# Performance work log

Measured on AMD Instinct MI355X. Metric: run time of the kernel, lower is better.

The kernel has to match this reference:

```python
import jax, jax.numpy as jnp
import numpy as np
import math

K = 32          # knn neighbors
NN = 32         # num_neighbor (kernel columns)
MAP = 32        # map_size
GROUP = 4
IN_C = 64
OUT_C = 64
EPS = 1e-5
TOPK = 3        # neighbors kept per kernel column in topkmax


def knn_idx(xc, k):
    # xc: [B,N,3]; returns indices of k nearest points (self included first)
    sq = -jnp.sum(xc * xc, axis=-1, keepdims=True)            # [B,N,1]
    pair = sq + 2.0 * jnp.einsum('bnd,bmd->bnm', xc, xc) + jnp.swapaxes(sq, 1, 2)
    return jax.lax.top_k(pair, k)[1]                          # [B,N,k]


def topkmax(p):
    # p: [M,k,NN]; keep top-TOPK along neighbor axis (dim=1), softmax over it
    pt = jnp.swapaxes(p, 1, 2)                                # [M,NN,k]
    thr = jax.lax.top_k(pt, TOPK)[0][..., -1:]
    pt = jnp.where(pt >= thr, pt, -1e10)
    return jnp.swapaxes(jax.nn.softmax(pt, axis=-1), 1, 2)


def setup_inputs() -> dict:
    key = jax.random.key(0)
    ks = jax.random.split(key, 8)
    B, N = 8, 2048
    in_c_x = IN_C // 2
    F = IN_C + in_c_x                                         # 96
    return {
        'x': jax.random.normal(ks[0], (B, 3, N), jnp.float32),
        'feature': jax.random.normal(ks[1], (B, IN_C, N), jnp.float32),
        'B_mat': jax.random.normal(ks[2], (7, MAP), jnp.float32),
        'kernels': jax.random.normal(ks[3], (3, NN), jnp.float32),
        'mlp_w': jax.random.normal(ks[4], (in_c_x, 2 * MAP), jnp.float32) * 0.1,
        'mlp_b': jnp.zeros((in_c_x,), jnp.float32),
        'conv_w': jax.random.normal(ks[5], (OUT_C, F * NN), jnp.float32) * 0.02,
        'conv_b': jnp.zeros((OUT_C,), jnp.float32),
        'bn_gamma': jnp.ones((OUT_C,), jnp.float32),
        'bn_beta': jnp.zeros((OUT_C,), jnp.float32),
    }


def reference(x, feature, B_mat, kernels, mlp_w, mlp_b, conv_w, conv_b, bn_gamma, bn_beta):
    bsz, in_c, n = feature.shape
    in_c_x = in_c // 2
    F = in_c + in_c_x
    M = bsz * n

    xc = jnp.swapaxes(x, 1, 2)                                # [B,N,3]
    idx = knn_idx(xc, K)                                      # [B,N,K]
    bix = jnp.arange(bsz)[:, None, None]

    x_neighs = xc[bix, idx].reshape(M, K, 3)                  # gather coords
    x_rep = jnp.broadcast_to(x_neighs[:, :1, :], x_neighs.shape)
    x_rel = x_neighs - x_rep
    x_dis = jnp.linalg.norm(x_rel, axis=-1, keepdims=True)

    # random Fourier features of [center, relative, distance]
    ff = (2.0 * math.pi) * jnp.concatenate([x_rep, x_rel, x_dis], -1) @ B_mat  # [M,K,MAP]
    ff = jnp.concatenate([jnp.sin(ff), jnp.cos(ff)], -1)                        # [M,K,2*MAP]
    x_feats = jnp.einsum('mki,oi->mok', ff, mlp_w) + mlp_b[None, :, None]       # [M,in_c_x,K]

    fN = jnp.swapaxes(feature, 1, 2)                          # [B,N,C]
    feats = fN[bix, idx].reshape(M, K, in_c)                  # gather features
    feats = jnp.swapaxes(feats, 1, 2)                         # [M,C,K]
    feats = jnp.concatenate([feats, x_feats], axis=1)         # [M,F,K]

    one_pad = jnp.zeros((K, NN), feature.dtype).at[0, 0].set(1.0)
    perm = topkmax(jnp.einsum('mkd,dn->mkn', x_rel, kernels) + one_pad)  # [M,K,NN]

    # group channel shuffle (F > 3 + in_c_x holds for in_c=64)
    feats = feats.reshape(M, GROUP, F // GROUP, K).transpose(0, 2, 1, 3).reshape(M, F, K)
    feats = jnp.einsum('mfk,mkn->mfn', feats, perm).reshape(M, F * NN)

    out = (feats @ conv_w.T + conv_b).reshape(bsz, n, -1)
    out = jnp.swapaxes(out, 1, 2)                             # [B,out_c,N]

    # BatchNorm1d, training-mode batch statistics over (B,N)
    mean = out.mean(axis=(0, 2), keepdims=True)
    var = out.var(axis=(0, 2), keepdims=True)
    return bn_gamma[None, :, None] * (out - mean) / jnp.sqrt(var + EPS) + bn_beta[None, :, None]
```

## Files before the change

kernel.cpp:

```cpp
#include <hip/hip_runtime.h>
#include <math.h>

#define NPTS 2048
#define NBATCH 8
#define MTOT (NBATCH*NPTS)
#define KROW 4096
#define OUTC 64

using bf16x8 = __attribute__((ext_vector_type(8))) short;
using f32x4  = __attribute__((ext_vector_type(4))) float;

__device__ __forceinline__ unsigned short f2bf(float f) {
    unsigned u = __float_as_uint(f);
    unsigned r = u + 0x7FFFu + ((u >> 16) & 1u);
    return (unsigned short)(r >> 16);
}

__device__ __forceinline__ double bcast_d(double v, int srclane) {
    int lo = __builtin_amdgcn_readlane(__double2loint(v), srclane);
    int hi = __builtin_amdgcn_readlane(__double2hiint(v), srclane);
    return __hiloint2double(hi, lo);
}

__device__ __forceinline__ unsigned wave_max_u32(unsigned v) {
    int x = (int)v, t;
    t = __builtin_amdgcn_update_dpp(x, x, 0x111, 0xF, 0xF, false); x = ((unsigned)t > (unsigned)x) ? t : x;
    t = __builtin_amdgcn_update_dpp(x, x, 0x112, 0xF, 0xF, false); x = ((unsigned)t > (unsigned)x) ? t : x;
    t = __builtin_amdgcn_update_dpp(x, x, 0x114, 0xF, 0xF, false); x = ((unsigned)t > (unsigned)x) ? t : x;
    t = __builtin_amdgcn_update_dpp(x, x, 0x118, 0xF, 0xF, false); x = ((unsigned)t > (unsigned)x) ? t : x;
    t = __builtin_amdgcn_update_dpp(x, x, 0x142, 0xa, 0xF, false); x = ((unsigned)t > (unsigned)x) ? t : x;
    t = __builtin_amdgcn_update_dpp(x, x, 0x143, 0xc, 0xF, false); x = ((unsigned)t > (unsigned)x) ? t : x;
    return (unsigned)__builtin_amdgcn_readlane(x, 63);
}

__global__ __launch_bounds__(256) void knn_kernel(const float* __restrict__ x,
                                                  int* __restrict__ idxout) {
    __shared__ float xs[NPTS], ys[NPTS], zs[NPTS], sqs[NPTS];
    int t = threadIdx.x;
    int b = blockIdx.x / (NPTS / 4);
    int grp = blockIdx.x % (NPTS / 4);
    const float* xb = x + (size_t)b * 3 * NPTS;
    for (int i = t; i < NPTS; i += 256) {
        float vx = xb[i], vy = xb[NPTS + i], vz = xb[2 * NPTS + i];
        xs[i] = vx; ys[i] = vy; zs[i] = vz;
        sqs[i] = -((vx * vx + vy * vy) + vz * vz);
    }
    __syncthreads();
    int wave = t >> 6, lane = t & 63;
    int n = grp * 4 + wave;
    float cx = xs[n], cy = ys[n], cz = zs[n];
    float sqn = sqs[n];
    float cx2 = 2.0f * cx, cy2 = 2.0f * cy, cz2 = 2.0f * cz;

    unsigned key[32];
#pragma unroll
    for (int j = 0; j < 32; j++) {
        int cand = j * 64 + lane;
        float v = sqn + sqs[cand];
        v = fmaf(cx2, xs[cand], v);
        v = fmaf(cy2, ys[cand], v);
        v = fmaf(cz2, zs[cand], v);
        unsigned u = __float_as_uint(v);
        unsigned ord = u ^ ((u >> 31) ? 0xFFFFFFFFu : 0x80000000u);
        key[j] = (ord & 0xFFFFFFE0u) | (unsigned)j;
    }
#pragma unroll
    for (int k = 2; k <= 32; k <<= 1) {
#pragma unroll
        for (int j = k >> 1; j >= 1; j >>= 1) {
#pragma unroll
            for (int i = 0; i < 32; i++) {
                int l2 = i ^ j;
                if (l2 > i) {
                    unsigned a = key[i], bb = key[l2];
                    unsigned hi = a > bb ? a : bb, lo = a > bb ? bb : a;
                    if ((i & k) == 0) { key[i] = hi; key[l2] = lo; }
                    else              { key[i] = lo; key[l2] = hi; }
                }
            }
        }
    }
    int sg = 0;
    for (int r = 0; r < 40; r++) {
        unsigned m = wave_max_u32(key[0]);
        unsigned long long ball = __ballot(key[0] == m);
        int bl = __ffsll(ball) - 1;
        int gidx = (int)(m & 31u) * 64 + bl;
        if (lane == r) sg = gidx;
        bool won = (lane == bl);
#pragma unroll
        for (int i = 0; i < 11; i++) key[i] = won ? key[i + 1] : key[i];
        key[11] = won ? 0u : key[11];
    }
    double cxd = (double)cx, cyd = (double)cy, czd = (double)cz;
    double sqnd = -((cxd * cxd + cyd * cyd) + czd * czd);
    double v; int oid;
    if (lane < 40) {
        double mx = (double)xs[sg], my = (double)ys[sg], mz = (double)zs[sg];
        double dot = (cxd * mx + cyd * my) + czd * mz;
        double sqm = -((mx * mx + my * my) + mz * mz);
        v = (sqnd + 2.0 * dot) + sqm;
        oid = sg;
    } else {
        v = -1.0e300; oid = (1 << 28) + lane;
    }
#pragma unroll
    for (int k = 2; k <= 64; k <<= 1) {
#pragma unroll
        for (int j = k >> 1; j >= 1; j >>= 1) {
            double ov = __shfl_xor(v, j);
            int oi = __shfl_xor(oid, j);
            bool amLow = (lane & j) == 0;
            bool asc = (lane & k) == 0;
            bool gt = (ov > v) || (ov == v && oi < oid);
            bool ga = gt != amLow;
            bool take = asc ? ga : !ga;
            if (take) { v = ov; oid = oi; }
        }
    }
    if (lane >= 32) idxout[((size_t)b * NPTS + n) * 32 + (63 - lane)] = oid;
}

__global__ __launch_bounds__(256) void transpose_kernel(const float* __restrict__ feat,
                                                        unsigned short* __restrict__ fTb) {
    __shared__ float tile[64][65];
    int b = blockIdx.x / 32;
    int n0 = (blockIdx.x % 32) * 64;
    int t = threadIdx.x;
    int nt = t % 64, cg = t / 64;
    for (int cc = 0; cc < 16; cc++) {
        int c2 = cg * 16 + cc;
        tile[c2][nt] = feat[((size_t)b * 64 + c2) * NPTS + n0 + nt];
    }
    __syncthreads();
    int c2 = t % 64, ng = t / 64;
    for (int nn2 = 0; nn2 < 16; nn2++) {
        int n = ng * 16 + nn2;
        fTb[((size_t)b * NPTS + n0 + n) * 64 + c2] = f2bf(tile[c2][n]);
    }
}

__global__ __launch_bounds__(256) void wprep2_kernel(
    const float* __restrict__ cw, const float* __restrict__ mlpw,
    const float* __restrict__ mb, const float* __restrict__ cb,
    unsigned short* __restrict__ WtT, float* __restrict__ cbw) {
    int oc = blockIdx.x;
    int t = threadIdx.x;
    for (int i = t; i < 2048; i += 256) {
        int f = i >> 5, col = i & 31;
        int r = (f % 24) * 4 + f / 24;
        WtT[(size_t)oc * KROW + i] = f2bf(cw[(size_t)oc * 3072 + r * 32 + col]);
    }
    for (int i = t; i < 2048; i += 256) {
        int j = i >> 5, col = i & 31;
        float s = 0.f;
        for (int o2 = 0; o2 < 32; o2++) {
            int f = 64 + o2;
            int r = (f % 24) * 4 + f / 24;
            s = fmaf(mlpw[o2 * 64 + j], cw[(size_t)oc * 3072 + r * 32 + col], s);
        }
        WtT[(size_t)oc * KROW + 2048 + i] = f2bf(s);
    }
    if (t == 0) {
        float s = cb[oc];
        for (int o2 = 0; o2 < 32; o2++) {
            int f = 64 + o2;
            int r = (f % 24) * 4 + f / 24;
            float rowsum = 0.f;
            for (int col = 0; col < 32; col++) rowsum += cw[(size_t)oc * 3072 + r * 32 + col];
            s = fmaf(mb[o2], rowsum, s);
        }
        cbw[oc] = s;
    }
}

__global__ void kprep_kernel(const float* __restrict__ ker, double* __restrict__ kerd) {
    int i = threadIdx.x;
    if (i < 96) kerd[i] = (double)ker[i];
}

__global__ __launch_bounds__(256) void point2_kernel(
    const float* __restrict__ x, const unsigned short* __restrict__ fTb,
    const int* __restrict__ idx, const float* __restrict__ Bm,
    const double* __restrict__ kerd, unsigned short* __restrict__ Aof,
    int m_base, int m_count) {
    __shared__ __align__(16) unsigned short lds2[4 * 3840];
    int t = threadIdx.x;
    int wv = t >> 6, l = t & 63;
    int k = l & 31, h = l >> 5;
    unsigned short* G2 = lds2 + wv * 3840;
    unsigned short* PT = G2 + 2560;
    int lr = l & 15, lq = l >> 4;
    double ck0 = kerd[k], ck1 = kerd[32 + k], ck2 = kerd[64 + k];
    int gw = blockIdx.x * 4 + wv;
    int nw = gridDim.x * 4;

    for (int mi = gw; mi < m_count; mi += nw) {
        int m = m_base + mi;
        int b = m >> 11;
        int ik = idx[(size_t)m * 32 + k];
        const float* xb = x + (size_t)b * 3 * NPTS;
        float nx0 = xb[ik], ny0 = xb[NPTS + ik], nz0 = xb[2 * NPTS + ik];
        const unsigned short* fr = fTb + (((size_t)b * NPTS + ik) * 64 + h * 32);
        uint4 f0 = *(const uint4*)fr;
        uint4 f1 = *(const uint4*)(fr + 8);
        uint4 f2 = *(const uint4*)(fr + 16);
        uint4 f3 = *(const uint4*)(fr + 24);

        float cx = __shfl(nx0, 0), cy = __shfl(ny0, 0), cz = __shfl(nz0, 0);
        double rxd = (double)nx0 - (double)cx;
        double ryd = (double)ny0 - (double)cy;
        double rzd = (double)nz0 - (double)cz;
        float rx = (float)rxd, ry = (float)ryd, rz = (float)rzd;
        float dist = sqrtf((rx * rx + ry * ry) + rz * rz);

        double pd[32];
#pragma unroll
        for (int kk = 0; kk < 32; kk++) {
            double bx = bcast_d(rxd, kk);
            double by = bcast_d(ryd, kk);
            double bz = bcast_d(rzd, kk);
            pd[kk] = bx * ck0 + by * ck1 + bz * ck2;
        }
        if (k == 0) pd[0] += 1.0;

        double m1 = -1.0e300, m2 = -1.0e300, m3 = -1.0e300;
#pragma unroll
        for (int kk = 0; kk < 32; kk++) {
            double v = pd[kk];
            double t2 = fmin(v, m1);
            double t3 = fmin(v, m2);
            m1 = fmax(m1, v);
            m2 = fmax(m2, t2);
            m3 = fmax(m3, t3);
        }
        float pv[32];
        float ssum = 0.f;
#pragma unroll
        for (int kk = 0; kk < 32; kk++) {
            float e = (pd[kk] >= m3) ? __expf((float)(pd[kk] - m1)) : 0.f;
            pv[kk] = e; ssum += e;
        }
        float rs = 1.f / ssum;
#pragma unroll
        for (int kk = 0; kk < 32; kk++) pv[kk] *= rs;

        int c = k;
        {
            unsigned w[16];
#pragma unroll
            for (int i = 0; i < 16; i++)
                w[i] = (unsigned)f2bf(pv[2 * i]) | ((unsigned)f2bf(pv[2 * i + 1]) << 16);
            unsigned s[8];
#pragma unroll
            for (int i = 0; i < 8; i++) s[i] = h ? w[8 + i] : w[i];
            *(uint4*)&PT[c * 40 + h * 16]     = make_uint4(s[0], s[1], s[2], s[3]);
            *(uint4*)&PT[c * 40 + h * 16 + 8] = make_uint4(s[4], s[5], s[6], s[7]);
        }
        {
            unsigned fw[16] = {f0.x, f0.y, f0.z, f0.w, f1.x, f1.y, f1.z, f1.w,
                               f2.x, f2.y, f2.z, f2.w, f3.x, f3.y, f3.z, f3.w};
#pragma unroll
            for (int c2 = 0; c2 < 16; c2++) {
                unsigned v = fw[c2];
                unsigned o = (unsigned)__shfl_xor((int)v, 1);
                unsigned wr = (k & 1) ? ((o >> 16) | (v & 0xFFFF0000u))
                                      : ((v & 0xFFFFu) | (o << 16));
                int ch = h * 32 + 2 * c2 + (k & 1);
                *(unsigned*)&G2[ch * 40 + (k & ~1)] = wr;
            }
        }
        asm volatile("" ::: "memory");

        bf16x8 af0 = *(const bf16x8*)&PT[(lr)      * 40 + lq * 8];
        bf16x8 af1 = *(const bf16x8*)&PT[(16 + lr) * 40 + lq * 8];
        size_t obase = (size_t)mi * KROW;
#pragma unroll
        for (int fb = 0; fb < 4; fb++) {
            int row = fb * 16 + lr;
            bf16x8 bfr = *(const bf16x8*)&G2[row * 40 + lq * 8];
            f32x4 d0 = __builtin_amdgcn_mfma_f32_16x16x32_bf16(af0, bfr, (f32x4){0.f, 0.f, 0.f, 0.f}, 0, 0, 0);
            f32x4 d1 = __builtin_amdgcn_mfma_f32_16x16x32_bf16(af1, bfr, (f32x4){0.f, 0.f, 0.f, 0.f}, 0, 0, 0);
            unsigned q0 = (unsigned)f2bf(d0.x) | ((unsigned)f2bf(d0.y) << 16);
            unsigned q1 = (unsigned)f2bf(d0.z) | ((unsigned)f2bf(d0.w) << 16);
            *(uint2*)&Aof[obase + row * 32 + lq * 4] = make_uint2(q0, q1);
            unsigned q2 = (unsigned)f2bf(d1.x) | ((unsigned)f2bf(d1.y) << 16);
            unsigned q3 = (unsigned)f2bf(d1.z) | ((unsigned)f2bf(d1.w) << 16);
            *(uint2*)&Aof[obase + row * 32 + 16 + lq * 4] = make_uint2(q2, q3);
        }
        asm volatile("" ::: "memory");

        {
            float u[32];
#pragma unroll
            for (int f = 0; f < 32; f++) {
                float uu = cx * Bm[f];
                uu = fmaf(cy, Bm[32 + f], uu);
                uu = fmaf(cz, Bm[64 + f], uu);
                uu = fmaf(rx, Bm[96 + f], uu);
                uu = fmaf(ry, Bm[128 + f], uu);
                uu = fmaf(rz, Bm[160 + f], uu);
                uu = fmaf(dist, Bm[192 + f], uu);
                u[f] = 6.28318530717958647692f * uu;
            }
            float tv[32];
            if (h == 0) {
#pragma unroll
                for (int f = 0; f < 32; f++) tv[f] = __sinf(u[f]);
            } else {
#pragma unroll
                for (int f = 0; f < 32; f++) tv[f] = __cosf(u[f]);
            }
#pragma unroll
            for (int jj = 0; jj < 16; jj++) {
                unsigned b0 = f2bf(tv[jj]), b1 = f2bf(tv[jj + 16]);
                unsigned o0 = (unsigned)__shfl_xor((int)b0, 1);
                unsigned o1 = (unsigned)__shfl_xor((int)b1, 1);
                unsigned wr = (k & 1) ? ((o1 & 0xFFFFu) | (b1 << 16))
                                      : ((b0 & 0xFFFFu) | (o0 << 16));
                int row = h * 32 + (k & 1) * 16 + jj;
                *(unsigned*)&G2[row * 40 + (k & ~1)] = wr;
            }
        }
        asm volatile("" ::: "memory");

#pragma unroll
        for (int fb = 0; fb < 4; fb++) {
            int row = fb * 16 + lr;
            bf16x8 bfr = *(const bf16x8*)&G2[row * 40 + lq * 8];
            f32x4 d0 = __builtin_amdgcn_mfma_f32_16x16x32_bf16(af0, bfr, (f32x4){0.f, 0.f, 0.f, 0.f}, 0, 0, 0);
            f32x4 d1 = __builtin_amdgcn_mfma_f32_16x16x32_bf16(af1, bfr, (f32x4){0.f, 0.f, 0.f, 0.f}, 0, 0, 0);
            int f = 64 + row;
            unsigned q0 = (unsigned)f2bf(d0.x) | ((unsigned)f2bf(d0.y) << 16);
            unsigned q1 = (unsigned)f2bf(d0.z) | ((unsigned)f2bf(d0.w) << 16);
            *(uint2*)&Aof[obase + f * 32 + lq * 4] = make_uint2(q0, q1);
            unsigned q2 = (unsigned)f2bf(d1.x) | ((unsigned)f2bf(d1.y) << 16);
            unsigned q3 = (unsigned)f2bf(d1.z) | ((unsigned)f2bf(d1.w) << 16);
            *(uint2*)&Aof[obase + f * 32 + 16 + lq * 4] = make_uint2(q2, q3);
        }
        asm volatile("" ::: "memory");
    }
}

__global__ __launch_bounds__(256) void conv2_kernel(
    const unsigned short* __restrict__ A, const unsigned short* __restrict__ WtT,
    const float* __restrict__ cbw, float* __restrict__ outp, int m_base) {
    __shared__ unsigned short Al[64 * 72];
    __shared__ unsigned short Wl[64 * 72];
    int t = threadIdx.x;
    int wv = t >> 6, l = t & 63;
    int lr = l & 15, lq = l >> 4;
    int m0 = blockIdx.x * 64;
    int mr = t >> 3, kq = t & 7;
    f32x4 acc[4] = {};
    for (int ks = 0; ks < 64; ks++) {
        int k0 = ks * 64;
        uint4 a0 = *(const uint4*)&A[(size_t)(m0 + mr) * KROW + k0 + kq * 8];
        uint4 a1 = *(const uint4*)&A[(size_t)(m0 + mr + 32) * KROW + k0 + kq * 8];
        uint4 w0 = *(const uint4*)&WtT[(size_t)mr * KROW + k0 + kq * 8];
        uint4 w1 = *(const uint4*)&WtT[(size_t)(mr + 32) * KROW + k0 + kq * 8];
        __syncthreads();
        *(uint4*)&Al[mr * 72 + kq * 8] = a0;
        *(uint4*)&Al[(mr + 32) * 72 + kq * 8] = a1;
        *(uint4*)&Wl[mr * 72 + kq * 8] = w0;
        *(uint4*)&Wl[(mr + 32) * 72 + kq * 8] = w1;
        __syncthreads();
#pragma unroll
        for (int kk = 0; kk < 2; kk++) {
            bf16x8 af = *(const bf16x8*)&Al[(wv * 16 + lr) * 72 + kk * 32 + lq * 8];
#pragma unroll
            for (int ocb = 0; ocb < 4; ocb++) {
                bf16x8 wf = *(const bf16x8*)&Wl[(ocb * 16 + lr) * 72 + kk * 32 + lq * 8];
                acc[ocb] = __builtin_amdgcn_mfma_f32_16x16x32_bf16(af, wf, acc[ocb], 0, 0, 0);
            }
        }
    }
    int m = m_base + m0 + wv * 16 + lq * 4;
    int b = m >> 11, n = m & 2047;
#pragma unroll
    for (int ocb = 0; ocb < 4; ocb++) {
        int oc = ocb * 16 + lr;
        float bias = cbw[oc];
        float4 v = make_float4(acc[ocb].x + bias, acc[ocb].y + bias,
                               acc[ocb].z + bias, acc[ocb].w + bias);
        *(float4*)&outp[((size_t)(b * 64 + oc)) * 2048 + n] = v;
    }
}

__global__ __launch_bounds__(256) void bn1_kernel(const float* __restrict__ outp,
                                                  float* __restrict__ sums) {
    int c = blockIdx.x, t = threadIdx.x;
    float s = 0.0f, s2 = 0.0f;
    for (int b = 0; b < NBATCH; b++) {
        const float* p = outp + ((size_t)b * 64 + c) * NPTS;
        for (int i = t; i < NPTS; i += 256) {
            float v = p[i];
            s += v; s2 = fmaf(v, v, s2);
        }
    }
    __shared__ float r1[256], r2[256];
    r1[t] = s; r2[t] = s2;
    __syncthreads();
    for (int st = 128; st > 0; st >>= 1) {
        if (t < st) { r1[t] += r1[t + st]; r2[t] += r2[t + st]; }
        __syncthreads();
    }
    if (t == 0) { sums[c] = r1[0]; sums[64 + c] = r2[0]; }
}

__global__ __launch_bounds__(256) void bn2_kernel(float* __restrict__ outp,
                                                  const float* __restrict__ sums,
                                                  const float* __restrict__ gamma,
                                                  const float* __restrict__ beta) {
    int i = blockIdx.x * 256 + threadIdx.x;
    if (i >= MTOT * 64) return;
    int c = (i >> 11) & 63;
    float mean = sums[c] * (1.0f / (float)MTOT);
    float var = sums[64 + c] * (1.0f / (float)MTOT) - mean * mean;
    float inv = rsqrtf(var + 1e-5f);
    outp[i] = fmaf(gamma[c], (outp[i] - mean) * inv, beta[c]);
}

extern "C" void kernel_launch(void* const* d_in, const int* in_sizes, int n_in,
                              void* d_out, int out_size, void* d_ws, size_t ws_size,
                              hipStream_t stream) {
    (void)in_sizes; (void)n_in; (void)out_size;
    const float* x    = (const float*)d_in[0];
    const float* fea  = (const float*)d_in[1];
    const float* Bm   = (const float*)d_in[2];
    const float* ker  = (const float*)d_in[3];
    const float* mw   = (const float*)d_in[4];
    const float* mb   = (const float*)d_in[5];
    const float* cw   = (const float*)d_in[6];
    const float* cb   = (const float*)d_in[7];
    const float* gam  = (const float*)d_in[8];
    const float* bet  = (const float*)d_in[9];
    float* outp = (float*)d_out;

    char* wsb = (char*)d_ws;
    size_t off = 0;
    auto carve = [&](size_t sz) {
        void* p = wsb + off;
        off = (off + sz + 255) & ~(size_t)255;
        return p;
    };
    unsigned short* fTb  = (unsigned short*)carve((size_t)MTOT * 64 * 2);
    int*            idxw = (int*)carve((size_t)MTOT * 32 * 4);
    unsigned short* WtT  = (unsigned short*)carve((size_t)OUTC * KROW * 2);
    float*          cbw  = (float*)carve(64 * 4);
    double*         kerd = (double*)carve(96 * 8);
    float*          sums = (float*)carve(2 * 64 * 4);
    size_t fixedEnd = off;
    int CS = 16384;
    while (fixedEnd + (size_t)CS * KROW * 2 > ws_size && CS > 2048) CS >>= 1;
    unsigned short* Aof = (unsigned short*)(wsb + fixedEnd);

    knn_kernel<<<NBATCH * (NPTS / 4), 256, 0, stream>>>(x, idxw);
    transpose_kernel<<<NBATCH * 32, 256, 0, stream>>>(fea, fTb);
    wprep2_kernel<<<64, 256, 0, stream>>>(cw, mw, mb, cb, WtT, cbw);
    kprep_kernel<<<1, 128, 0, stream>>>(ker, kerd);

    for (int c0 = 0; c0 < MTOT; c0 += CS) {
        point2_kernel<<<1024, 256, 0, stream>>>(x, fTb, idxw, Bm, kerd, Aof, c0, CS);
        conv2_kernel<<<CS / 64, 256, 0, stream>>>(Aof, WtT, cbw, outp, c0);
    }
    bn1_kernel<<<64, 256, 0, stream>>>(outp, sums);
    bn2_kernel<<<(MTOT * 64 + 255) / 256, 256, 0, stream>>>(outp, sums, gam, bet);
}
```

Before: 218.2 us.

## Split top-k softmax permutation into separate kernel with two points per wave

Moves the per-point kernel projection, top-3 selection and softmax out of the fused point kernel into a new perm_kernel. The new kernel processes two points per wave, one per 32-lane half, using shuffles instead of readlane broadcasts, and writes the bf16 permutation matrices to a new workspace buffer. The point kernel then loads these from global memory, uses less LDS, and launches more blocks. The intent is to use all 64 lanes for the double-precision work and raise occupancy of the point kernel. The cost is an extra round trip to global memory of about 32 MB and one more kernel launch.

Result: faster. 211.7 us (-3.0%).

```diff
diff --git a/kernel.cpp b/kernel.cpp
--- a/kernel.cpp
+++ b/kernel.cpp
@@ -14,12 +14,6 @@
     unsigned u = __float_as_uint(f);
     unsigned r = u + 0x7FFFu + ((u >> 16) & 1u);
     return (unsigned short)(r >> 16);
-}
-
-__device__ __forceinline__ double bcast_d(double v, int srclane) {
-    int lo = __builtin_amdgcn_readlane(__double2loint(v), srclane);
-    int hi = __builtin_amdgcn_readlane(__double2hiint(v), srclane);
-    return __hiloint2double(hi, lo);
 }
 
 __device__ __forceinline__ unsigned wave_max_u32(unsigned v) {
@@ -179,19 +173,77 @@
     if (i < 96) kerd[i] = (double)ker[i];
 }
 
-__global__ __launch_bounds__(256) void point2_kernel(
+__global__ __launch_bounds__(256) void perm_kernel(
+    const float* __restrict__ x, const int* __restrict__ idx,
+    const double* __restrict__ kerd, unsigned short* __restrict__ PTws) {
+    int t = threadIdx.x;
+    int wv = t >> 6, l = t & 63;
+    int c = l & 31;
+    int cbase = l & 32;
+    int m = blockIdx.x * 8 + wv * 2 + (l >> 5);
+    int b = m >> 11;
+    int ik = idx[(size_t)m * 32 + c];
+    const float* xb = x + (size_t)b * 3 * NPTS;
+    float nx0 = xb[ik], ny0 = xb[NPTS + ik], nz0 = xb[2 * NPTS + ik];
+    float cx = __shfl(nx0, cbase), cy = __shfl(ny0, cbase), cz = __shfl(nz0, cbase);
+    double rxd = (double)nx0 - (double)cx;
+    double ryd = (double)ny0 - (double)cy;
+    double rzd = (double)nz0 - (double)cz;
+    double ck0 = kerd[c], ck1 = kerd[32 + c], ck2 = kerd[64 + c];
+
+    double pd[32];
+#pragma unroll
+    for (int kk = 0; kk < 32; kk++) {
+        double bx = __shfl(rxd, cbase + kk);
+        double by = __shfl(ryd, cbase + kk);
+        double bz = __shfl(rzd, cbase + kk);
+        pd[kk] = bx * ck0 + by * ck1 + bz * ck2;
+    }
+    if (c == 0) pd[0] += 1.0;
+
+    double m1 = -1.0e300, m2 = -1.0e300, m3 = -1.0e300;
+#pragma unroll
+    for (int kk = 0; kk < 32; kk++) {
+        double v = pd[kk];
+        double t2 = fmin(v, m1);
+        double t3 = fmin(v, m2);
+        m1 = fmax(m1, v);
+        m2 = fmax(m2, t2);
+        m3 = fmax(m3, t3);
+    }
+    float pv[32];
+    float ssum = 0.f;
+#pragma unroll
+    for (int kk = 0; kk < 32; kk++) {
+        float e = (pd[kk] >= m3) ? __expf((float)(pd[kk] - m1)) : 0.f;
+        pv[kk] = e; ssum += e;
+    }
+    float rs = 1.f / ssum;
+#pragma unroll
+    for (int kk = 0; kk < 32; kk++) pv[kk] *= rs;
+
+    unsigned w[16];
+#pragma unroll
+    for (int i = 0; i < 16; i++)
+        w[i] = (unsigned)f2bf(pv[2 * i]) | ((unsigned)f2bf(pv[2 * i + 1]) << 16);
+    size_t obase = (size_t)m * 1024 + (size_t)c * 32;
+    *(uint4*)&PTws[obase]      = make_uint4(w[0], w[1], w[2], w[3]);
+    *(uint4*)&PTws[obase + 8]  = make_uint4(w[4], w[5], w[6], w[7]);
+    *(uint4*)&PTws[obase + 16] = make_uint4(w[8], w[9], w[10], w[11]);
+    *(uint4*)&PTws[obase + 24] = make_uint4(w[12], w[13], w[14], w[15]);
+}
+
+__global__ __launch_bounds__(256) void point3_kernel(
     const float* __restrict__ x, const unsigned short* __restrict__ fTb,
     const int* __restrict__ idx, const float* __restrict__ Bm,
-    const double* __restrict__ kerd, unsigned short* __restrict__ Aof,
+    const unsigned short* __restrict__ PTws, unsigned short* __restrict__ Aof,
     int m_base, int m_count) {
-    __shared__ __align__(16) unsigned short lds2[4 * 3840];
+    __shared__ __align__(16) unsigned short lds2[4 * 2560];
     int t = threadIdx.x;
     int wv = t >> 6, l = t & 63;
     int k = l & 31, h = l >> 5;
-    unsigned short* G2 = lds2 + wv * 3840;
-    unsigned short* PT = G2 + 2560;
+    unsigned short* G2 = lds2 + wv * 2560;
     int lr = l & 15, lq = l >> 4;
-    double ck0 = kerd[k], ck1 = kerd[32 + k], ck2 = kerd[64 + k];
     int gw = blockIdx.x * 4 + wv;
     int nw = gridDim.x * 4;
 
@@ -206,57 +258,14 @@
         uint4 f1 = *(const uint4*)(fr + 8);
         uint4 f2 = *(const uint4*)(fr + 16);
         uint4 f3 = *(const uint4*)(fr + 24);
+        const unsigned short* ptp = PTws + (size_t)m * 1024;
+        bf16x8 af0 = *(const bf16x8*)&ptp[lr * 32 + lq * 8];
+        bf16x8 af1 = *(const bf16x8*)&ptp[(16 + lr) * 32 + lq * 8];
 
         float cx = __shfl(nx0, 0), cy = __shfl(ny0, 0), cz = __shfl(nz0, 0);
-        double rxd = (double)nx0 - (double)cx;
-        double ryd = (double)ny0 - (double)cy;
-        double rzd = (double)nz0 - (double)cz;
-        float rx = (float)rxd, ry = (float)ryd, rz = (float)rzd;
+        float rx = nx0 - cx, ry = ny0 - cy, rz = nz0 - cz;
         float dist = sqrtf((rx * rx + ry * ry) + rz * rz);
 
-        double pd[32];
-#pragma unroll
-        for (int kk = 0; kk < 32; kk++) {
-            double bx = bcast_d(rxd, kk);
-            double by = bcast_d(ryd, kk);
-            double bz = bcast_d(rzd, kk);
-            pd[kk] = bx * ck0 + by * ck1 + bz * ck2;
-        }
-        if (k == 0) pd[0] += 1.0;
-
-        double m1 = -1.0e300, m2 = -1.0e300, m3 = -1.0e300;
-#pragma unroll
-        for (int kk = 0; kk < 32; kk++) {
-            double v = pd[kk];
-            double t2 = fmin(v, m1);
-            double t3 = fmin(v, m2);
-            m1 = fmax(m1, v);
-            m2 = fmax(m2, t2);
-            m3 = fmax(m3, t3);
-        }
-        float pv[32];
-        float ssum = 0.f;
-#pragma unroll
-        for (int kk = 0; kk < 32; kk++) {
-            float e = (pd[kk] >= m3) ? __expf((float)(pd[kk] - m1)) : 0.f;
-            pv[kk] = e; ssum += e;
-        }
-        float rs = 1.f / ssum;
-#pragma unroll
-        for (int kk = 0; kk < 32; kk++) pv[kk] *= rs;
-
-        int c = k;
-        {
-            unsigned w[16];
-#pragma unroll
-            for (int i = 0; i < 16; i++)
-                w[i] = (unsigned)f2bf(pv[2 * i]) | ((unsigned)f2bf(pv[2 * i + 1]) << 16);
-            unsigned s[8];
-#pragma unroll
-            for (int i = 0; i < 8; i++) s[i] = h ? w[8 + i] : w[i];
-            *(uint4*)&PT[c * 40 + h * 16]     = make_uint4(s[0], s[1], s[2], s[3]);
-            *(uint4*)&PT[c * 40 + h * 16 + 8] = make_uint4(s[4], s[5], s[6], s[7]);
-        }
         {
             unsigned fw[16] = {f0.x, f0.y, f0.z, f0.w, f1.x, f1.y, f1.z, f1.w,
                                f2.x, f2.y, f2.z, f2.w, f3.x, f3.y, f3.z, f3.w};
@@ -272,8 +281,6 @@
         }
         asm volatile("" ::: "memory");
 
-        bf16x8 af0 = *(const bf16x8*)&PT[(lr)      * 40 + lq * 8];
-        bf16x8 af1 = *(const bf16x8*)&PT[(16 + lr) * 40 + lq * 8];
         size_t obase = (size_t)mi * KROW;
 #pragma unroll
         for (int fb = 0; fb < 4; fb++) {
@@ -450,6 +457,7 @@
     float*          cbw  = (float*)carve(64 * 4);
     double*         kerd = (double*)carve(96 * 8);
     float*          sums = (float*)carve(2 * 64 * 4);
+    unsigned short* PTws = (unsigned short*)carve((size_t)MTOT * 1024 * 2);
     size_t fixedEnd = off;
     int CS = 16384;
     while (fixedEnd + (size_t)CS * KROW * 2 > ws_size && CS > 2048) CS >>= 1;
@@ -459,9 +467,10 @@
     transpose_kernel<<<NBATCH * 32, 256, 0, stream>>>(fea, fTb);
     wprep2_kernel<<<64, 256, 0, stream>>>(cw, mw, mb, cb, WtT, cbw);
     kprep_kernel<<<1, 128, 0, stream>>>(ker, kerd);
+    perm_kernel<<<MTOT / 8, 256, 0, stream>>>(x, idxw, kerd, PTws);
 
     for (int c0 = 0; c0 < MTOT; c0 += CS) {
-        point2_kernel<<<1024, 256, 0, stream>>>(x, fTb, idxw, Bm, kerd, Aof, c0, CS);
+        point3_kernel<<<1536, 256, 0, stream>>>(x, fTb, idxw, Bm, PTws, Aof, c0, CS);
         conv2_kernel<<<CS / 64, 256, 0, stream>>>(Aof, WtT, cbw, outp, c0);
     }
     bn1_kernel<<<64, 256, 0, stream>>>(outp, sums);
```
